# Kernel tuning notes

Measured on AMD Instinct MI355X. Metric: run time of the kernel, lower is better.

The kernel has to match this reference:

```python
import jax, jax.numpy as jnp
import numpy as np

B, S, D_MODEL, H = 4, 1024, 1024, 16
DEPTH = D_MODEL // H


def head_scales():
    # np.arange(0.1, 10 + 0.01, 9.9 / (H - 1)) -> exactly H values from 0.1 to 10.0
    return jnp.asarray(np.arange(0.1, 10 + 0.01, 9.9 / (H - 1)), dtype=jnp.float32)


def setup_inputs() -> dict:
    key = jax.random.key(0)
    ks = jax.random.split(key, 14)
    sd = 1.0 / np.sqrt(D_MODEL)
    inp = {
        "v": jax.random.normal(ks[0], (B, S, D_MODEL), jnp.float32),
        "k": jax.random.normal(ks[1], (B, S, D_MODEL), jnp.float32),
        "q": jax.random.normal(ks[2], (B, S, D_MODEL), jnp.float32),
        # pairwise distance-like weights in [0, 1)
        "weight": jax.random.uniform(ks[3], (B, S, S), jnp.float32),
        # binary padding mask, broadcastable to (B, H, S, S); 1 = masked
        "mask": (jax.random.uniform(ks[4], (B, 1, 1, S)) < 0.1).astype(jnp.float32),
        "Wq": jax.random.normal(ks[5], (D_MODEL, D_MODEL), jnp.float32) * sd,
        "bq": jnp.zeros((D_MODEL,), jnp.float32),
        "Wk": jax.random.normal(ks[6], (D_MODEL, D_MODEL), jnp.float32) * sd,
        "bk": jnp.zeros((D_MODEL,), jnp.float32),
        "Wv": jax.random.normal(ks[7], (D_MODEL, D_MODEL), jnp.float32) * sd,
        "bv": jnp.zeros((D_MODEL,), jnp.float32),
        "Wo": jax.random.normal(ks[8], (D_MODEL, D_MODEL), jnp.float32) * sd,
        "bo": jnp.zeros((D_MODEL,), jnp.float32),
    }
    return inp


def reference(v, k, q, weight, mask, Wq, bq, Wk, bk, Wv, bv, Wo, bo):
    def split_heads(x):  # (B, S, D) -> (B, H, S, depth)
        return x.reshape(B, -1, H, DEPTH).transpose(0, 2, 1, 3)

    qh = split_heads(q @ Wq + bq)
    kh = split_heads(k @ Wk + bk)
    vh = split_heads(v @ Wv + bv)

    # shift_distance[b,h,i,j] = weight[b,i,j] * scale[h]
    scales = head_scales()  # (H,)
    bias = weight[:, None, :, :] * scales[None, :, None, None]  # (B, H, S, S)

    logits = jnp.einsum("bhqd,bhkd->bhqk", qh, kh) / jnp.sqrt(
        jnp.asarray(DEPTH, jnp.float32)
    )
    logits = logits + bias + mask * (-1e9)
    attn = jax.nn.softmax(logits, axis=-1)  # (B, H, S, S)
    out = jnp.einsum("bhqk,bhkd->bhqd", attn, vh)  # (B, H, S, depth)
    out = out.transpose(0, 2, 1, 3).reshape(B, -1, D_MODEL)
    return out @ Wo + bo
```

## Files before the change

### kernel.cpp

```cpp
#include <hip/hip_runtime.h>
#include <hip/hip_fp16.h>

#define DEV __device__ __forceinline__

typedef _Float16 f16x8 __attribute__((ext_vector_type(8)));
typedef float f32x4 __attribute__((ext_vector_type(4)));

DEV void gload16(void* lds, const void* g) {
  __builtin_amdgcn_global_load_lds((__attribute__((address_space(1))) const void*)g,
                                   (__attribute__((address_space(3))) void*)lds,
                                   16, 0, 0);
}

DEV f32x4 mfma16(f16x8 a, f16x8 b, f32x4 c) {
  return __builtin_amdgcn_mfma_f32_16x16x32_f16(a, b, c, 0, 0, 0);
}

__global__ __launch_bounds__(256) void transw_kernel(
    const float* __restrict__ W0, const float* __restrict__ W1,
    const float* __restrict__ W2, const float* __restrict__ W3,
    _Float16* __restrict__ Wt) {
  __shared__ float tile[32][33];
  const float* W = (blockIdx.z == 0) ? W0 : (blockIdx.z == 1) ? W1
                 : (blockIdx.z == 2) ? W2 : W3;
  _Float16* dst = Wt + (size_t)blockIdx.z * (1024 * 1024);
  const int tx = threadIdx.x & 31, ty = threadIdx.x >> 5;
  const int n0 = blockIdx.x * 32, k0 = blockIdx.y * 32;
#pragma unroll
  for (int i = 0; i < 4; ++i)
    tile[ty + i * 8][tx] = W[(size_t)(k0 + ty + i * 8) * 1024 + n0 + tx];
  __syncthreads();
#pragma unroll
  for (int i = 0; i < 4; ++i)
    dst[(size_t)(n0 + ty + i * 8) * 1024 + k0 + tx] = (_Float16)tile[tx][ty + i * 8];
}

__global__ __launch_bounds__(256) void wcast_kernel(const float* __restrict__ W,
                                                    _Float16* __restrict__ Wh) {
  const size_t i = (size_t)(blockIdx.x * 256 + threadIdx.x) * 8;
  float4 a = *(const float4*)(W + i);
  float4 b = *(const float4*)(W + i + 4);
  f16x8 o;
  o[0] = (_Float16)a.x; o[1] = (_Float16)a.y; o[2] = (_Float16)a.z; o[3] = (_Float16)a.w;
  o[4] = (_Float16)b.x; o[5] = (_Float16)b.y; o[6] = (_Float16)b.z; o[7] = (_Float16)b.w;
  *(f16x8*)(Wh + i) = o;
}

__global__ __launch_bounds__(256) void qkvcast_kernel(
    const float* __restrict__ q, const float* __restrict__ k,
    const float* __restrict__ v, _Float16* __restrict__ Ah) {
  const float* src = (blockIdx.y == 0) ? q : (blockIdx.y == 1) ? k : v;
  _Float16* dst = Ah + (size_t)blockIdx.y * (4096ull * 1024);
  const size_t i = (size_t)(blockIdx.x * 256 + threadIdx.x) * 8;
  float4 a = *(const float4*)(src + i);
  float4 b = *(const float4*)(src + i + 4);
  f16x8 o;
  o[0] = (_Float16)a.x; o[1] = (_Float16)a.y; o[2] = (_Float16)a.z; o[3] = (_Float16)a.w;
  o[4] = (_Float16)b.x; o[5] = (_Float16)b.y; o[6] = (_Float16)b.z; o[7] = (_Float16)b.w;
  *(f16x8*)(dst + i) = o;
}

template <bool AF32>
DEV void gemm_core(const void* __restrict__ Aptr, const _Float16* __restrict__ Bt,
                   _Float16* Al, _Float16* Bl, int m0, int n0, f32x4 (&acc)[4][4]) {
  const int t = threadIdx.x;
  const int l = t & 63, w = t >> 6;
  const int wr = w >> 1, wc = w & 1;
  const int lo = l & 15, lg = l >> 4;

  for (int ks = 0; ks < 1024; ks += 32) {
    __syncthreads();
    gload16(&Bl[t * 8], Bt + (size_t)(n0 + (t >> 2)) * 1024 + ks + (t & 3) * 8);
    gload16(&Bl[(t + 256) * 8], Bt + (size_t)(n0 + (t >> 2) + 64) * 1024 + ks + (t & 3) * 8);
    if constexpr (AF32) {
      const float* Ag = (const float*)Aptr;
      const int row = t >> 1, c0 = (t & 1) * 16;
      const float4* src = (const float4*)(Ag + (size_t)(m0 + row) * 1024 + ks + c0);
      float4 f0 = src[0], f1 = src[1], f2 = src[2], f3 = src[3];
      f16x8 v0, v1;
      v0[0] = (_Float16)f0.x; v0[1] = (_Float16)f0.y; v0[2] = (_Float16)f0.z; v0[3] = (_Float16)f0.w;
      v0[4] = (_Float16)f1.x; v0[5] = (_Float16)f1.y; v0[6] = (_Float16)f1.z; v0[7] = (_Float16)f1.w;
      v1[0] = (_Float16)f2.x; v1[1] = (_Float16)f2.y; v1[2] = (_Float16)f2.z; v1[3] = (_Float16)f2.w;
      v1[4] = (_Float16)f3.x; v1[5] = (_Float16)f3.y; v1[6] = (_Float16)f3.z; v1[7] = (_Float16)f3.w;
      *(f16x8*)&Al[row * 32 + c0] = v0;
      *(f16x8*)&Al[row * 32 + c0 + 8] = v1;
    } else {
      const _Float16* Ag = (const _Float16*)Aptr;
      gload16(&Al[t * 8], Ag + (size_t)(m0 + (t >> 2)) * 1024 + ks + (t & 3) * 8);
      gload16(&Al[(t + 256) * 8], Ag + (size_t)(m0 + (t >> 2) + 64) * 1024 + ks + (t & 3) * 8);
    }
    __syncthreads();

    f16x8 af[4], bf[4];
#pragma unroll
    for (int mi = 0; mi < 4; ++mi)
      af[mi] = *(const f16x8*)&Al[(wr * 64 + mi * 16 + lo) * 32 + lg * 8];
#pragma unroll
    for (int ni = 0; ni < 4; ++ni)
      bf[ni] = *(const f16x8*)&Bl[(wc * 64 + ni * 16 + lo) * 32 + lg * 8];
#pragma unroll
    for (int mi = 0; mi < 4; ++mi)
#pragma unroll
      for (int ni = 0; ni < 4; ++ni)
        acc[mi][ni] = mfma16(af[mi], bf[ni], acc[mi][ni]);
  }
}

template <bool AHALF>
__global__ __launch_bounds__(256) void proj_kernel(
    const _Float16* __restrict__ Ah, const float* __restrict__ qin,
    const float* __restrict__ kin, const float* __restrict__ vin,
    const _Float16* __restrict__ Wt, const float* __restrict__ bq,
    const float* __restrict__ bk, const float* __restrict__ bv,
    _Float16* __restrict__ Qh, _Float16* __restrict__ Kt,
    _Float16* __restrict__ Vt) {
  __shared__ __attribute__((aligned(16))) _Float16 Al[128 * 32];
  __shared__ __attribute__((aligned(16))) _Float16 Bl[128 * 32];
  const int lin = blockIdx.x + (blockIdx.y << 3) + (blockIdx.z << 8);
  const int work = (lin & 7) * 96 + (lin >> 3);
  const int z = work >> 8;
  const int m0 = ((work & 255) >> 3) * 128;
  const int n0 = (work & 7) * 128;

  const _Float16* Bt = Wt + (size_t)z * (1 << 20);
  const float* bias = (z == 0) ? bq : (z == 1) ? bk : bv;
  _Float16* C = (z == 0) ? Qh : (z == 1) ? Kt : Vt;

  f32x4 acc[4][4];
#pragma unroll
  for (int i = 0; i < 4; ++i)
#pragma unroll
    for (int j = 0; j < 4; ++j) acc[i][j] = (f32x4){0.f, 0.f, 0.f, 0.f};
  if constexpr (AHALF) {
    gemm_core<false>(Ah + (size_t)z * (4096ull * 1024), Bt, Al, Bl, m0, n0, acc);
  } else {
    const float* A = (z == 0) ? qin : (z == 1) ? kin : vin;
    gemm_core<true>(A, Bt, Al, Bl, m0, n0, acc);
  }

  const int l = threadIdx.x & 63, w = threadIdx.x >> 6;
  const int wr = w >> 1, wc = w & 1;
  const int lo = l & 15, lg = l >> 4;
#pragma unroll
  for (int mi = 0; mi < 4; ++mi) {
#pragma unroll
    for (int ni = 0; ni < 4; ++ni) {
      const int col = n0 + wc * 64 + ni * 16 + lo;
      const int rowb = m0 + wr * 64 + mi * 16 + lg * 4;
      const float bc = bias[col];
      const int h = col >> 6, d = col & 63;
#pragma unroll
      for (int r = 0; r < 4; ++r) {
        const float vv = acc[mi][ni][r] + bc;
        const int m = rowb + r;
        const int b = m >> 10, s = m & 1023;
        const size_t slab = (size_t)(b * 16 + h) * 65536;
        if (z == 0) {
          C[slab + (size_t)s * 64 + d] = (_Float16)vv;
        } else if (z == 1) {
          C[slab + (size_t)(s >> 6) * 4096 + (size_t)(s & 63) * 64 +
            (((d >> 3) ^ (s & 7)) << 3) + (d & 7)] = (_Float16)vv;
        } else {
          C[slab + (size_t)(s >> 6) * 4096 + (size_t)d * 64 +
            ((((s >> 3) & 7) ^ (d & 7)) << 3) + (s & 7)] = (_Float16)vv;
        }
      }
    }
  }
}

__global__ __launch_bounds__(256) void outproj_kernel(
    const _Float16* __restrict__ AO, const _Float16* __restrict__ Bt,
    const float* __restrict__ bias, float* __restrict__ out) {
  __shared__ __attribute__((aligned(16))) _Float16 Al[128 * 32];
  __shared__ __attribute__((aligned(16))) _Float16 Bl[128 * 32];
  const int lin = blockIdx.x + (blockIdx.y << 3);
  const int work = (lin & 7) * 32 + (lin >> 3);
  const int m0 = (work >> 3) * 128;
  const int n0 = (work & 7) * 128;
  f32x4 acc[4][4];
#pragma unroll
  for (int i = 0; i < 4; ++i)
#pragma unroll
    for (int j = 0; j < 4; ++j) acc[i][j] = (f32x4){0.f, 0.f, 0.f, 0.f};
  gemm_core<false>(AO, Bt, Al, Bl, m0, n0, acc);

  const int l = threadIdx.x & 63, w = threadIdx.x >> 6;
  const int wr = w >> 1, wc = w & 1;
  const int lo = l & 15, lg = l >> 4;
#pragma unroll
  for (int mi = 0; mi < 4; ++mi) {
#pragma unroll
    for (int ni = 0; ni < 4; ++ni) {
      const int col = n0 + wc * 64 + ni * 16 + lo;
      const int rowb = m0 + wr * 64 + mi * 16 + lg * 4;
      const float bc = bias[col];
#pragma unroll
      for (int r = 0; r < 4; ++r)
        out[(size_t)(rowb + r) * 1024 + col] = acc[mi][ni][r] + bc;
    }
  }
}

__global__ __launch_bounds__(512, 4) void attn_kernel(
    const _Float16* __restrict__ Qh, const _Float16* __restrict__ Kt,
    const _Float16* __restrict__ Vt, const _Float16* __restrict__ Wh,
    const float* __restrict__ mask, _Float16* __restrict__ AO) {
  __shared__ __attribute__((aligned(16))) _Float16 Kl[2][4096];
  __shared__ __attribute__((aligned(16))) _Float16 Vl[2][4096];
  __shared__ __attribute__((aligned(16))) _Float16 Pl[8][16][72];
  const int t = threadIdx.x, l = t & 63, w = t >> 6;
  const int lo = l & 15, lg = l >> 4;
  const int bh = blockIdx.y, b = bh >> 4, h = bh & 15;
  const int q0w = blockIdx.x * 128 + w * 16;
  constexpr float L2E = 1.44269504089f;
  const float scale = 0.1f + (float)h * (9.9f / 15.0f);
  const float cS = 0.125f * L2E;
  const float cW = scale * L2E;
  const float cM = -1e9f * L2E;
  const _Float16* Kslab = Kt + (size_t)bh * 65536;
  const _Float16* Vslab = Vt + (size_t)bh * 65536;
  const _Float16* Wb = Wh + ((size_t)b << 20);
  const float* Mb = mask + (size_t)b * 1024;
  const int qrow = q0w + lg * 4;

  const f16x8 qf0 = *(const f16x8*)(Qh + (size_t)bh * 65536 + (q0w + lo) * 64 + lg * 8);
  const f16x8 qf1 = *(const f16x8*)(Qh + (size_t)bh * 65536 + (q0w + lo) * 64 + 32 + lg * 8);

  f32x4 oacc[4];
#pragma unroll
  for (int di = 0; di < 4; ++di) oacc[di] = (f32x4){0.f, 0.f, 0.f, 0.f};
  float mrun[4], lsum[4];
#pragma unroll
  for (int r = 0; r < 4; ++r) { mrun[r] = -1e38f; lsum[r] = 0.f; }

  gload16(&Kl[0][t * 8], Kslab + t * 8);
  gload16(&Vl[0][t * 8], Vslab + t * 8);
  __syncthreads();

  for (int kt = 0; kt < 16; ++kt) {
    const int cur = kt & 1;
    if (kt + 1 < 16) {
      gload16(&Kl[cur ^ 1][t * 8], Kslab + (size_t)(kt + 1) * 4096 + t * 8);
      gload16(&Vl[cur ^ 1][t * 8], Vslab + (size_t)(kt + 1) * 4096 + t * 8);
    }
    const int kv0 = kt * 64;
    const _Float16* Kb = Kl[cur];
    const _Float16* Vb = Vl[cur];
    const int sl = lg ^ (lo & 7);

    float sv[4][4];
    float tm[4] = {-1e38f, -1e38f, -1e38f, -1e38f};
#pragma unroll
    for (int ni = 0; ni < 4; ++ni) {
      const int key = kv0 + ni * 16 + lo;
      const float mkv = Mb[key] * cM;
      float wgt[4];
#pragma unroll
      for (int r = 0; r < 4; ++r)
        wgt[r] = (float)Wb[(size_t)(qrow + r) * 1024 + key];
      const int kr = ni * 16 + lo;
      f16x8 kf0 = *(const f16x8*)(Kb + kr * 64 + sl * 8);
      f16x8 kf1 = *(const f16x8*)(Kb + kr * 64 + (sl ^ 4) * 8);
      f32x4 s = (f32x4){0.f, 0.f, 0.f, 0.f};
      s = mfma16(qf0, kf0, s);
      s = mfma16(qf1, kf1, s);
#pragma unroll
      for (int r = 0; r < 4; ++r) {
        const float x = s[r] * cS + wgt[r] * cW + mkv;
        sv[ni][r] = x;
        tm[r] = fmaxf(tm[r], x);
      }
    }
#pragma unroll
    for (int st = 1; st < 16; st <<= 1)
#pragma unroll
      for (int r = 0; r < 4; ++r) tm[r] = fmaxf(tm[r], __shfl_xor(tm[r], st));
    float fr[4];
#pragma unroll
    for (int r = 0; r < 4; ++r) {
      const float mn = fmaxf(mrun[r], tm[r]);
      fr[r] = exp2f(mrun[r] - mn);
      mrun[r] = mn;
      lsum[r] *= fr[r];
    }
#pragma unroll
    for (int di = 0; di < 4; ++di)
#pragma unroll
      for (int r = 0; r < 4; ++r) oacc[di][r] *= fr[r];
#pragma unroll
    for (int ni = 0; ni < 4; ++ni)
#pragma unroll
      for (int r = 0; r < 4; ++r) {
        const float p = exp2f(sv[ni][r] - mrun[r]);
        lsum[r] += p;
        Pl[w][lg * 4 + r][ni * 16 + lo] = (_Float16)p;
      }
    const f16x8 pa0 = *(const f16x8*)(&Pl[w][lo][lg * 8]);
    const f16x8 pa1 = *(const f16x8*)(&Pl[w][lo][32 + lg * 8]);
    __builtin_amdgcn_s_setprio(1);
#pragma unroll
    for (int di = 0; di < 4; ++di) {
      const int d = di * 16 + lo;
      f16x8 vf0 = *(const f16x8*)(Vb + d * 64 + sl * 8);
      f16x8 vf1 = *(const f16x8*)(Vb + d * 64 + (sl ^ 4) * 8);
      oacc[di] = mfma16(pa0, vf0, oacc[di]);
      oacc[di] = mfma16(pa1, vf1, oacc[di]);
    }
    __builtin_amdgcn_s_setprio(0);
    __syncthreads();
  }

#pragma unroll
  for (int st = 1; st < 16; st <<= 1)
#pragma unroll
    for (int r = 0; r < 4; ++r) lsum[r] += __shfl_xor(lsum[r], st);
#pragma unroll
  for (int r = 0; r < 4; ++r) {
    const float inv = 1.0f / lsum[r];
#pragma unroll
    for (int di = 0; di < 4; ++di)
      AO[((size_t)(b * 1024) + qrow + r) * 1024 + h * 64 + di * 16 + lo] =
          (_Float16)(oacc[di][r] * inv);
  }
}

extern "C" void kernel_launch(void* const* d_in, const int* in_sizes, int n_in,
                              void* d_out, int out_size, void* d_ws, size_t ws_size,
                              hipStream_t stream) {
  (void)in_sizes; (void)n_in; (void)out_size;
  const float* v      = (const float*)d_in[0];
  const float* k      = (const float*)d_in[1];
  const float* q      = (const float*)d_in[2];
  const float* weight = (const float*)d_in[3];
  const float* mask   = (const float*)d_in[4];
  const float* Wq = (const float*)d_in[5];
  const float* bq = (const float*)d_in[6];
  const float* Wk = (const float*)d_in[7];
  const float* bk = (const float*)d_in[8];
  const float* Wv = (const float*)d_in[9];
  const float* bv = (const float*)d_in[10];
  const float* Wo = (const float*)d_in[11];
  const float* bo = (const float*)d_in[12];
  float* out = (float*)d_out;

  const size_t MB = 1ull << 20;
  char* ws = (char*)d_ws;
  _Float16* Wt = (_Float16*)ws;
  _Float16* Qh = (_Float16*)(ws + 8 * MB);
  _Float16* Kt = (_Float16*)(ws + 16 * MB);
  _Float16* Vt = (_Float16*)(ws + 24 * MB);
  _Float16* Wh = (_Float16*)(ws + 32 * MB);
  _Float16* AO = (_Float16*)(ws + 40 * MB);
  _Float16* Ah = (_Float16*)(ws + 40 * MB);

  transw_kernel<<<dim3(32, 32, 4), 256, 0, stream>>>(Wq, Wk, Wv, Wo, Wt);
  wcast_kernel<<<2048, 256, 0, stream>>>(weight, Wh);
  if (ws_size >= 64 * MB) {
    qkvcast_kernel<<<dim3(2048, 3), 256, 0, stream>>>(q, k, v, Ah);
    proj_kernel<true><<<dim3(8, 32, 3), 256, 0, stream>>>(Ah, q, k, v, Wt, bq, bk, bv,
                                                          Qh, Kt, Vt);
  } else {
    proj_kernel<false><<<dim3(8, 32, 3), 256, 0, stream>>>(nullptr, q, k, v, Wt, bq, bk,
                                                           bv, Qh, Kt, Vt);
  }
  attn_kernel<<<dim3(8, 64), 512, 0, stream>>>(Qh, Kt, Vt, Wh, mask, AO);
  outproj_kernel<<<dim3(8, 32), 256, 0, stream>>>(AO, Wt + 3 * (1 << 20), bo, out);
}
```

Measured before the change: 153.3 us.

## Split attention over key halves with merge kernel, lazy rescale, fused input cast

Attention is split into two key-range halves via a grid z dimension, doubling block count, and a merge kernel combines the partial outputs using stored (max, sum) statistics. The online-softmax rescale is skipped when the running max grows by at most 8 (log2 units) across the wavefront. The separate q/k/v fp16 cast kernel is removed so projection always converts fp32 in-kernel, with the LDS A stride padded to 40 to reduce bank conflicts. The gains are more parallelism and fewer launches, paid for with extra partial-output traffic, an additional merge launch, and reuse of the Qh buffer as the attention output.

Measured after the change: 154.4 us. Within noise of the previous version (+0.7%).

```diff
diff --git a/kernel.cpp b/kernel.cpp
--- a/kernel.cpp
+++ b/kernel.cpp
@@ -4,6 +4,7 @@
 #define DEV __device__ __forceinline__
 
 typedef _Float16 f16x8 __attribute__((ext_vector_type(8)));
+typedef _Float16 f16x4 __attribute__((ext_vector_type(4)));
 typedef float f32x4 __attribute__((ext_vector_type(4)));
 
 DEV void gload16(void* lds, const void* g) {
@@ -46,23 +47,10 @@
   *(f16x8*)(Wh + i) = o;
 }
 
-__global__ __launch_bounds__(256) void qkvcast_kernel(
-    const float* __restrict__ q, const float* __restrict__ k,
-    const float* __restrict__ v, _Float16* __restrict__ Ah) {
-  const float* src = (blockIdx.y == 0) ? q : (blockIdx.y == 1) ? k : v;
-  _Float16* dst = Ah + (size_t)blockIdx.y * (4096ull * 1024);
-  const size_t i = (size_t)(blockIdx.x * 256 + threadIdx.x) * 8;
-  float4 a = *(const float4*)(src + i);
-  float4 b = *(const float4*)(src + i + 4);
-  f16x8 o;
-  o[0] = (_Float16)a.x; o[1] = (_Float16)a.y; o[2] = (_Float16)a.z; o[3] = (_Float16)a.w;
-  o[4] = (_Float16)b.x; o[5] = (_Float16)b.y; o[6] = (_Float16)b.z; o[7] = (_Float16)b.w;
-  *(f16x8*)(dst + i) = o;
-}
-
 template <bool AF32>
 DEV void gemm_core(const void* __restrict__ Aptr, const _Float16* __restrict__ Bt,
                    _Float16* Al, _Float16* Bl, int m0, int n0, f32x4 (&acc)[4][4]) {
+  constexpr int AS = AF32 ? 40 : 32;
   const int t = threadIdx.x;
   const int l = t & 63, w = t >> 6;
   const int wr = w >> 1, wc = w & 1;
@@ -82,8 +70,8 @@
       v0[4] = (_Float16)f1.x; v0[5] = (_Float16)f1.y; v0[6] = (_Float16)f1.z; v0[7] = (_Float16)f1.w;
       v1[0] = (_Float16)f2.x; v1[1] = (_Float16)f2.y; v1[2] = (_Float16)f2.z; v1[3] = (_Float16)f2.w;
       v1[4] = (_Float16)f3.x; v1[5] = (_Float16)f3.y; v1[6] = (_Float16)f3.z; v1[7] = (_Float16)f3.w;
-      *(f16x8*)&Al[row * 32 + c0] = v0;
-      *(f16x8*)&Al[row * 32 + c0 + 8] = v1;
+      *(f16x8*)&Al[row * AS + c0] = v0;
+      *(f16x8*)&Al[row * AS + c0 + 8] = v1;
     } else {
       const _Float16* Ag = (const _Float16*)Aptr;
       gload16(&Al[t * 8], Ag + (size_t)(m0 + (t >> 2)) * 1024 + ks + (t & 3) * 8);
@@ -94,7 +82,7 @@
     f16x8 af[4], bf[4];
 #pragma unroll
     for (int mi = 0; mi < 4; ++mi)
-      af[mi] = *(const f16x8*)&Al[(wr * 64 + mi * 16 + lo) * 32 + lg * 8];
+      af[mi] = *(const f16x8*)&Al[(wr * 64 + mi * 16 + lo) * AS + lg * 8];
 #pragma unroll
     for (int ni = 0; ni < 4; ++ni)
       bf[ni] = *(const f16x8*)&Bl[(wc * 64 + ni * 16 + lo) * 32 + lg * 8];
@@ -106,15 +94,13 @@
   }
 }
 
-template <bool AHALF>
 __global__ __launch_bounds__(256) void proj_kernel(
-    const _Float16* __restrict__ Ah, const float* __restrict__ qin,
-    const float* __restrict__ kin, const float* __restrict__ vin,
-    const _Float16* __restrict__ Wt, const float* __restrict__ bq,
-    const float* __restrict__ bk, const float* __restrict__ bv,
-    _Float16* __restrict__ Qh, _Float16* __restrict__ Kt,
-    _Float16* __restrict__ Vt) {
-  __shared__ __attribute__((aligned(16))) _Float16 Al[128 * 32];
+    const float* __restrict__ qin, const float* __restrict__ kin,
+    const float* __restrict__ vin, const _Float16* __restrict__ Wt,
+    const float* __restrict__ bq, const float* __restrict__ bk,
+    const float* __restrict__ bv, _Float16* __restrict__ Qh,
+    _Float16* __restrict__ Kt, _Float16* __restrict__ Vt) {
+  __shared__ __attribute__((aligned(16))) _Float16 Al[128 * 40];
   __shared__ __attribute__((aligned(16))) _Float16 Bl[128 * 32];
   const int lin = blockIdx.x + (blockIdx.y << 3) + (blockIdx.z << 8);
   const int work = (lin & 7) * 96 + (lin >> 3);
@@ -122,6 +108,7 @@
   const int m0 = ((work & 255) >> 3) * 128;
   const int n0 = (work & 7) * 128;
 
+  const float* A = (z == 0) ? qin : (z == 1) ? kin : vin;
   const _Float16* Bt = Wt + (size_t)z * (1 << 20);
   const float* bias = (z == 0) ? bq : (z == 1) ? bk : bv;
   _Float16* C = (z == 0) ? Qh : (z == 1) ? Kt : Vt;
@@ -131,12 +118,7 @@
   for (int i = 0; i < 4; ++i)
 #pragma unroll
     for (int j = 0; j < 4; ++j) acc[i][j] = (f32x4){0.f, 0.f, 0.f, 0.f};
-  if constexpr (AHALF) {
-    gemm_core<false>(Ah + (size_t)z * (4096ull * 1024), Bt, Al, Bl, m0, n0, acc);
-  } else {
-    const float* A = (z == 0) ? qin : (z == 1) ? kin : vin;
-    gemm_core<true>(A, Bt, Al, Bl, m0, n0, acc);
-  }
+  gemm_core<true>(A, Bt, Al, Bl, m0, n0, acc);
 
   const int l = threadIdx.x & 63, w = threadIdx.x >> 6;
   const int wr = w >> 1, wc = w & 1;
@@ -202,10 +184,12 @@
   }
 }
 
+template <int NSPLIT>
 __global__ __launch_bounds__(512, 4) void attn_kernel(
     const _Float16* __restrict__ Qh, const _Float16* __restrict__ Kt,
     const _Float16* __restrict__ Vt, const _Float16* __restrict__ Wh,
-    const float* __restrict__ mask, _Float16* __restrict__ AO) {
+    const float* __restrict__ mask, void* __restrict__ Oout,
+    float2* __restrict__ Sst) {
   __shared__ __attribute__((aligned(16))) _Float16 Kl[2][4096];
   __shared__ __attribute__((aligned(16))) _Float16 Vl[2][4096];
   __shared__ __attribute__((aligned(16))) _Float16 Pl[8][16][72];
@@ -213,6 +197,9 @@
   const int lo = l & 15, lg = l >> 4;
   const int bh = blockIdx.y, b = bh >> 4, h = bh & 15;
   const int q0w = blockIdx.x * 128 + w * 16;
+  const int sp = (NSPLIT > 1) ? blockIdx.z : 0;
+  constexpr int NKT = 16 / NSPLIT;
+  const int kt0 = sp * NKT;
   constexpr float L2E = 1.44269504089f;
   const float scale = 0.1f + (float)h * (9.9f / 15.0f);
   const float cS = 0.125f * L2E;
@@ -223,6 +210,7 @@
   const _Float16* Wb = Wh + ((size_t)b << 20);
   const float* Mb = mask + (size_t)b * 1024;
   const int qrow = q0w + lg * 4;
+  const int sl = lg ^ (lo & 7);
 
   const f16x8 qf0 = *(const f16x8*)(Qh + (size_t)bh * 65536 + (q0w + lo) * 64 + lg * 8);
   const f16x8 qf1 = *(const f16x8*)(Qh + (size_t)bh * 65536 + (q0w + lo) * 64 + 32 + lg * 8);
@@ -234,20 +222,20 @@
 #pragma unroll
   for (int r = 0; r < 4; ++r) { mrun[r] = -1e38f; lsum[r] = 0.f; }
 
-  gload16(&Kl[0][t * 8], Kslab + t * 8);
-  gload16(&Vl[0][t * 8], Vslab + t * 8);
+  gload16(&Kl[0][t * 8], Kslab + (size_t)kt0 * 4096 + t * 8);
+  gload16(&Vl[0][t * 8], Vslab + (size_t)kt0 * 4096 + t * 8);
   __syncthreads();
 
-  for (int kt = 0; kt < 16; ++kt) {
-    const int cur = kt & 1;
-    if (kt + 1 < 16) {
+  for (int it = 0; it < NKT; ++it) {
+    const int kt = kt0 + it;
+    const int cur = it & 1;
+    if (it + 1 < NKT) {
       gload16(&Kl[cur ^ 1][t * 8], Kslab + (size_t)(kt + 1) * 4096 + t * 8);
       gload16(&Vl[cur ^ 1][t * 8], Vslab + (size_t)(kt + 1) * 4096 + t * 8);
     }
     const int kv0 = kt * 64;
     const _Float16* Kb = Kl[cur];
     const _Float16* Vb = Vl[cur];
-    const int sl = lg ^ (lo & 7);
 
     float sv[4][4];
     float tm[4] = {-1e38f, -1e38f, -1e38f, -1e38f};
@@ -276,18 +264,23 @@
     for (int st = 1; st < 16; st <<= 1)
 #pragma unroll
       for (int r = 0; r < 4; ++r) tm[r] = fmaxf(tm[r], __shfl_xor(tm[r], st));
-    float fr[4];
-#pragma unroll
-    for (int r = 0; r < 4; ++r) {
-      const float mn = fmaxf(mrun[r], tm[r]);
-      fr[r] = exp2f(mrun[r] - mn);
-      mrun[r] = mn;
-      lsum[r] *= fr[r];
-    }
-#pragma unroll
-    for (int di = 0; di < 4; ++di)
-#pragma unroll
-      for (int r = 0; r < 4; ++r) oacc[di][r] *= fr[r];
+    float delta = tm[0] - mrun[0];
+#pragma unroll
+    for (int r = 1; r < 4; ++r) delta = fmaxf(delta, tm[r] - mrun[r]);
+    if (!__all(delta <= 8.0f)) {
+      float fr[4];
+#pragma unroll
+      for (int r = 0; r < 4; ++r) {
+        const float mn = fmaxf(mrun[r], tm[r]);
+        fr[r] = exp2f(mrun[r] - mn);
+        mrun[r] = mn;
+        lsum[r] *= fr[r];
+      }
+#pragma unroll
+      for (int di = 0; di < 4; ++di)
+#pragma unroll
+        for (int r = 0; r < 4; ++r) oacc[di][r] *= fr[r];
+    }
 #pragma unroll
     for (int ni = 0; ni < 4; ++ni)
 #pragma unroll
@@ -315,14 +308,58 @@
   for (int st = 1; st < 16; st <<= 1)
 #pragma unroll
     for (int r = 0; r < 4; ++r) lsum[r] += __shfl_xor(lsum[r], st);
-#pragma unroll
-  for (int r = 0; r < 4; ++r) {
-    const float inv = 1.0f / lsum[r];
-#pragma unroll
-    for (int di = 0; di < 4; ++di)
-      AO[((size_t)(b * 1024) + qrow + r) * 1024 + h * 64 + di * 16 + lo] =
-          (_Float16)(oacc[di][r] * inv);
-  }
+
+  if constexpr (NSPLIT > 1) {
+    if (lo == 0) {
+#pragma unroll
+      for (int r = 0; r < 4; ++r)
+        Sst[(size_t)sp * 65536 + bh * 1024 + qrow + r] = make_float2(mrun[r], lsum[r]);
+    }
+    _Float16* Op = (_Float16*)Oout + (size_t)sp * (64ull * 1024 * 64);
+#pragma unroll
+    for (int r = 0; r < 4; ++r) {
+      const float inv = 1.0f / lsum[r];
+#pragma unroll
+      for (int di = 0; di < 4; ++di)
+        Op[((size_t)bh * 1024 + qrow + r) * 64 + di * 16 + lo] =
+            (_Float16)(oacc[di][r] * inv);
+    }
+  } else {
+    _Float16* AO = (_Float16*)Oout;
+#pragma unroll
+    for (int r = 0; r < 4; ++r) {
+      const float inv = 1.0f / lsum[r];
+#pragma unroll
+      for (int di = 0; di < 4; ++di)
+        AO[((size_t)(b * 1024) + qrow + r) * 1024 + h * 64 + di * 16 + lo] =
+            (_Float16)(oacc[di][r] * inv);
+    }
+  }
+}
+
+__global__ __launch_bounds__(256) void merge_kernel(
+    const _Float16* __restrict__ Op, const float2* __restrict__ Sst,
+    _Float16* __restrict__ AO) {
+  const int idx = blockIdx.x * 256 + threadIdx.x;
+  const int dc = idx & 15;
+  const int qq = (idx >> 4) & 1023;
+  const int bh = idx >> 14;
+  const int b = bh >> 4, h = bh & 15;
+  const float2 s1 = Sst[bh * 1024 + qq];
+  const float2 s2 = Sst[65536 + bh * 1024 + qq];
+  const float m = fmaxf(s1.x, s2.x);
+  float w1 = exp2f(s1.x - m) * s1.y;
+  float w2 = exp2f(s2.x - m) * s2.y;
+  const float inv = 1.f / (w1 + w2);
+  w1 *= inv; w2 *= inv;
+  const size_t o = ((size_t)bh * 1024 + qq) * 64 + dc * 4;
+  const f16x4 o1 = *(const f16x4*)(Op + o);
+  const f16x4 o2 = *(const f16x4*)(Op + (64ull * 1024 * 64) + o);
+  f16x4 r;
+#pragma unroll
+  for (int j = 0; j < 4; ++j)
+    r[j] = (_Float16)(w1 * (float)o1[j] + w2 * (float)o2[j]);
+  *(f16x4*)(AO + ((size_t)(b * 1024 + qq) * 1024 + h * 64 + dc * 4)) = r;
 }
 
 extern "C" void kernel_launch(void* const* d_in, const int* in_sizes, int n_in,
@@ -351,19 +388,21 @@
   _Float16* Kt = (_Float16*)(ws + 16 * MB);
   _Float16* Vt = (_Float16*)(ws + 24 * MB);
   _Float16* Wh = (_Float16*)(ws + 32 * MB);
-  _Float16* AO = (_Float16*)(ws + 40 * MB);
-  _Float16* Ah = (_Float16*)(ws + 40 * MB);
 
   transw_kernel<<<dim3(32, 32, 4), 256, 0, stream>>>(Wq, Wk, Wv, Wo, Wt);
   wcast_kernel<<<2048, 256, 0, stream>>>(weight, Wh);
-  if (ws_size >= 64 * MB) {
-    qkvcast_kernel<<<dim3(2048, 3), 256, 0, stream>>>(q, k, v, Ah);
-    proj_kernel<true><<<dim3(8, 32, 3), 256, 0, stream>>>(Ah, q, k, v, Wt, bq, bk, bv,
-                                                          Qh, Kt, Vt);
+  proj_kernel<<<dim3(8, 32, 3), 256, 0, stream>>>(q, k, v, Wt, bq, bk, bv, Qh, Kt, Vt);
+
+  if (ws_size >= 57 * MB) {
+    _Float16* Op  = (_Float16*)(ws + 40 * MB);
+    float2*   Sst = (float2*)(ws + 56 * MB);
+    _Float16* AO  = Qh;
+    attn_kernel<2><<<dim3(8, 64, 2), 512, 0, stream>>>(Qh, Kt, Vt, Wh, mask, Op, Sst);
+    merge_kernel<<<4096, 256, 0, stream>>>(Op, Sst, AO);
+    outproj_kernel<<<dim3(8, 32), 256, 0, stream>>>(AO, Wt + 3 * (1 << 20), bo, out);
   } else {
-    proj_kernel<false><<<dim3(8, 32, 3), 256, 0, stream>>>(nullptr, q, k, v, Wt, bq, bk,
-                                                           bv, Qh, Kt, Vt);
-  }
-  attn_kernel<<<dim3(8, 64), 512, 0, stream>>>(Qh, Kt, Vt, Wh, mask, AO);
-  outproj_kernel<<<dim3(8, 32), 256, 0, stream>>>(AO, Wt + 3 * (1 << 20), bo, out);
-}
+    _Float16* AO = (_Float16*)(ws + 40 * MB);
+    attn_kernel<1><<<dim3(8, 64, 1), 512, 0, stream>>>(Qh, Kt, Vt, Wh, mask, AO, nullptr);
+    outproj_kernel<<<dim3(8, 32), 256, 0, stream>>>(AO, Wt + 3 * (1 << 20), bo, out);
+  }
+}
```
